# Kernel optimization log

Measured on AMD Instinct MI355X. Metric: run time of the kernel, lower is better.

## Reference

```python
import jax, jax.numpy as jnp
import numpy as np

N_SVC, N_POD, N_NODE = 2000, 8000, 1000
T, F, H = 32, 64, 128
E_SVC, E_IN, E_NI = 30000, 24000, 24000


def setup_inputs() -> dict:
    key = jax.random.key(0)
    ks = jax.random.split(key, 32)
    s = 0.05
    inp = {
        'feat_svc': jax.random.normal(ks[0], (N_SVC, T, F), jnp.float32),
        'feat_pod': jax.random.normal(ks[1], (N_POD, T, F), jnp.float32),
        'feat_node': jax.random.normal(ks[2], (N_NODE, T, F), jnp.float32),
        # per-timestep GraphConv weights (one HGraphConvLayer per window step)
        'w_svc': jax.random.normal(ks[3], (T, F, H), jnp.float32) * s,
        'b_svc': jnp.zeros((T, H), jnp.float32),
        'w_in': jax.random.normal(ks[4], (T, F, H), jnp.float32) * s,   # pod -> node
        'b_in': jnp.zeros((T, H), jnp.float32),
        'w_ni': jax.random.normal(ks[5], (T, F, H), jnp.float32) * s,   # node -> pod
        'b_ni': jnp.zeros((T, H), jnp.float32),
        # per-timestep output linears (hidden -> 1) per node type
        'lw_svc': jax.random.normal(ks[6], (T, H), jnp.float32) * s,
        'lb_svc': jnp.zeros((T,), jnp.float32),
        'lw_pod': jax.random.normal(ks[7], (T, H), jnp.float32) * s,
        'lb_pod': jnp.zeros((T,), jnp.float32),
        'lw_node': jax.random.normal(ks[8], (T, H), jnp.float32) * s,
        'lb_node': jnp.zeros((T,), jnp.float32),
        # 2-layer LSTM (input_size = T = window_simple_size)
        'w_ih0': jax.random.normal(ks[9], (4 * H, T), jnp.float32) * s,
        'w_hh0': jax.random.normal(ks[10], (4 * H, H), jnp.float32) * s,
        'b_ih0': jnp.zeros((4 * H,), jnp.float32),
        'b_hh0': jnp.zeros((4 * H,), jnp.float32),
        'w_ih1': jax.random.normal(ks[11], (4 * H, H), jnp.float32) * s,
        'w_hh1': jax.random.normal(ks[12], (4 * H, H), jnp.float32) * s,
        'b_ih1': jnp.zeros((4 * H,), jnp.float32),
        'b_hh1': jnp.zeros((4 * H,), jnp.float32),
        # heterograph edge lists
        'e_svc_src': jax.random.randint(ks[13], (E_SVC,), 0, N_SVC, jnp.int64),
        'e_svc_dst': jax.random.randint(ks[14], (E_SVC,), 0, N_SVC, jnp.int64),
        'e_in_src': jax.random.randint(ks[15], (E_IN,), 0, N_POD, jnp.int64),
        'e_in_dst': jax.random.randint(ks[16], (E_IN,), 0, N_NODE, jnp.int64),
        'e_ni_src': jax.random.randint(ks[17], (E_NI,), 0, N_NODE, jnp.int64),
        'e_ni_dst': jax.random.randint(ks[18], (E_NI,), 0, N_POD, jnp.int64),
    }
    return inp


def _graph_conv(x, src, dst, n_dst, w, b):
    # DGL GraphConv, norm='both', batched over all T timesteps at once.
    # x: [N_src, T, F], w: [T, F, H], b: [T, H] -> [N_dst, T, H]
    n_src = x.shape[0]
    ones_e = jnp.ones(src.shape[0], x.dtype)
    out_deg = jnp.clip(jax.ops.segment_sum(ones_e, src, num_segments=n_src), 1.0)
    in_deg = jnp.clip(jax.ops.segment_sum(ones_e, dst, num_segments=n_dst), 1.0)
    xs = x * (out_deg ** -0.5)[:, None, None]
    agg = jax.ops.segment_sum(xs[src], dst, num_segments=n_dst)   # [N_dst, T, F]
    agg = agg * (in_deg ** -0.5)[:, None, None]
    return jnp.einsum('ntf,tfh->nth', agg, w) + b[None]


def _leaky(v):
    return jnp.where(v >= 0, v, 0.01 * v)


def _lstm(x, w_ih, w_hh, b_ih, b_hh):
    # unbatched LSTM over leading (node) axis; PyTorch gate order i,f,g,o
    Hh = w_hh.shape[1]
    b = b_ih + b_hh
    def step(carry, xt):
        h, c = carry
        g = xt @ w_ih.T + h @ w_hh.T + b
        i, f, gg, o = jnp.split(g, 4)
        i = jax.nn.sigmoid(i); f = jax.nn.sigmoid(f)
        gg = jnp.tanh(gg); o = jax.nn.sigmoid(o)
        c = f * c + i * gg
        h = o * jnp.tanh(c)
        return (h, c), h
    init = (jnp.zeros((Hh,), x.dtype), jnp.zeros((Hh,), x.dtype))
    _, ys = jax.lax.scan(step, init, x)
    return ys


def _forward(feat_svc, feat_pod, feat_node,
             w_svc, b_svc, w_in, b_in, w_ni, b_ni,
             lw_svc, lb_svc, lw_pod, lb_pod, lw_node, lb_node,
             w_ih0, w_hh0, b_ih0, b_hh0, w_ih1, w_hh1, b_ih1, b_hh1,
             e_svc_src, e_svc_dst, e_in_src, e_in_dst, e_ni_src, e_ni_dst):
    # HeteroGraphConv (sum aggregate; each dst type receives one edge type)
    h_svc = _graph_conv(feat_svc, e_svc_src, e_svc_dst, feat_svc.shape[0], w_svc, b_svc)
    h_node = _graph_conv(feat_pod, e_in_src, e_in_dst, feat_node.shape[0], w_in, b_in)
    h_pod = _graph_conv(feat_node, e_ni_src, e_ni_dst, feat_pod.shape[0], w_ni, b_ni)
    # per-timestep LeakyReLU + Linear(hidden -> 1), per node type
    s_svc = jnp.einsum('nth,th->nt', _leaky(h_svc), lw_svc) + lb_svc[None]
    s_pod = jnp.einsum('nth,th->nt', _leaky(h_pod), lw_pod) + lb_pod[None]
    s_node = jnp.einsum('nth,th->nt', _leaky(h_node), lw_node) + lb_node[None]
    x_seq = jnp.concatenate([s_svc, s_pod, s_node], axis=0)   # [N_total, T]
    # 2-layer LSTM over the node axis, input_size = T
    y = _lstm(x_seq, w_ih0, w_hh0, b_ih0, b_hh0)
    y = _lstm(y, w_ih1, w_hh1, b_ih1, b_hh1)
    return y   # [N_total, H]


def reference(feat_svc, feat_pod, feat_node,
              w_svc, b_svc, w_in, b_in, w_ni, b_ni,
              lw_svc, lb_svc, lw_pod, lb_pod, lw_node, lb_node,
              w_ih0, w_hh0, b_ih0, b_hh0, w_ih1, w_hh1, b_ih1, b_hh1,
              e_svc_src, e_svc_dst, e_in_src, e_in_dst, e_ni_src, e_ni_dst):
    return _forward(feat_svc, feat_pod, feat_node,
                    w_svc, b_svc, w_in, b_in, w_ni, b_ni,
                    lw_svc, lb_svc, lw_pod, lb_pod, lw_node, lb_node,
                    w_ih0, w_hh0, b_ih0, b_hh0, w_ih1, w_hh1, b_ih1, b_hh1,
                    e_svc_src, e_svc_dst, e_in_src, e_in_dst, e_ni_src, e_ni_dst)
```

## Files before the change

### kernel.cpp

```cpp
#include <hip/hip_runtime.h>

#define NSVC 2000
#define NPOD 8000
#define NNODE 1000
#define NTOT 11000
#define TT 32
#define FF 64
#define HH 128
#define EA 30000
#define EB 24000
#define EC 24000
#define ETOT (EA + EB + EC)
#define CHK 64
#define NCH ((NTOT + CHK - 1) / CHK)

__device__ __forceinline__ float ld_agent(const float* p) {
    return __hip_atomic_load(p, __ATOMIC_RELAXED, __HIP_MEMORY_SCOPE_AGENT);
}
__device__ __forceinline__ void st_agent(float* p, float v) {
    __hip_atomic_store(p, v, __ATOMIC_RELAXED, __HIP_MEMORY_SCOPE_AGENT);
}
__device__ __forceinline__ void bar_fast() {
    asm volatile("s_waitcnt lgkmcnt(0)" ::: "memory");
    __builtin_amdgcn_s_barrier();
}
template<int CTRL>
__device__ __forceinline__ float qperm(float x) {
    return __int_as_float(__builtin_amdgcn_mov_dpp(__float_as_int(x), CTRL, 0xF, 0xF, false));
}

__global__ void k_count3(const int* __restrict__ sA, const int* __restrict__ dA,
                         const int* __restrict__ sB, const int* __restrict__ dB,
                         const int* __restrict__ sC, const int* __restrict__ dC,
                         float* ocA, float* icA, float* ocB, float* icB,
                         float* ocC, float* icC) {
    int e = blockIdx.x * 256 + threadIdx.x;
    if (e < EA) {
        atomicAdd(ocA + sA[e], 1.f); atomicAdd(icA + dA[e], 1.f);
    } else if (e < EA + EB) {
        int i = e - EA;
        atomicAdd(ocB + sB[i], 1.f); atomicAdd(icB + dB[i], 1.f);
    } else if (e < ETOT) {
        int i = e - EA - EB;
        atomicAdd(ocC + sC[i], 1.f); atomicAdd(icC + dC[i], 1.f);
    }
}

__global__ void k_scan(const float* cA, int nA, int* oA,
                       const float* cB, int nB, int* oB,
                       const float* cC, int nC, int* oC) {
    const float* c; int n; int* o;
    if (blockIdx.x == 0)      { c = cA; n = nA; o = oA; }
    else if (blockIdx.x == 1) { c = cB; n = nB; o = oB; }
    else                      { c = cC; n = nC; o = oC; }
    __shared__ int s[256];
    __shared__ int carry;
    int tid = threadIdx.x;
    if (tid == 0) { carry = 0; o[0] = 0; }
    __syncthreads();
    for (int base = 0; base < n; base += 256) {
        int idx = base + tid;
        int v = (idx < n) ? (int)c[idx] : 0;
        s[tid] = v;
        __syncthreads();
        for (int d = 1; d < 256; d <<= 1) {
            int t = (tid >= d) ? s[tid - d] : 0;
            __syncthreads();
            s[tid] += t;
            __syncthreads();
        }
        if (idx < n) o[idx + 1] = carry + s[tid];
        __syncthreads();
        if (tid == 255) carry += s[255];
        __syncthreads();
    }
}

__global__ void k_scatter3(const int* __restrict__ sA, const int* __restrict__ dA,
                           const int* __restrict__ sB, const int* __restrict__ dB,
                           const int* __restrict__ sC, const int* __restrict__ dC,
                           const int* offA, int* curA, int* csrA,
                           const int* offB, int* curB, int* csrB,
                           const int* offC, int* curC, int* csrC) {
    int e = blockIdx.x * 256 + threadIdx.x;
    if (e < EA) {
        int d = dA[e]; int p = atomicAdd(curA + d, 1); csrA[offA[d] + p] = sA[e];
    } else if (e < EA + EB) {
        int i = e - EA;
        int d = dB[i]; int p = atomicAdd(curB + d, 1); csrB[offB[d] + p] = sB[i];
    } else if (e < ETOT) {
        int i = e - EA - EB;
        int d = dC[i]; int p = atomicAdd(curC + d, 1); csrC[offC[d] + p] = sC[i];
    }
}

#define YA16 ((NSVC + 15) / 16)
#define YC16 ((NPOD + 15) / 16)
#define YB16 ((NNODE + 15) / 16)
__global__ __launch_bounds__(256) void k_conv3(
    const float* __restrict__ feat_svc, const float* __restrict__ feat_pod,
    const float* __restrict__ feat_node,
    const float* __restrict__ w_svc, const float* __restrict__ b_svc,
    const float* __restrict__ lw_svc, const float* __restrict__ lb_svc,
    const float* __restrict__ w_ni, const float* __restrict__ b_ni,
    const float* __restrict__ lw_pod, const float* __restrict__ lb_pod,
    const float* __restrict__ w_in, const float* __restrict__ b_in,
    const float* __restrict__ lw_node, const float* __restrict__ lb_node,
    const float* ocA, const float* icA, const int* offA, const int* csrA,
    const float* ocC, const float* icC, const int* offC, const int* csrC,
    const float* ocB, const float* icB, const int* offB, const int* csrB,
    float* __restrict__ xseq)
{
    __shared__ float wl[FF * HH];
    __shared__ float bl[HH], lwl[HH];
    __shared__ float accs[4][FF];
    const int t = blockIdx.x;
    const int tid = threadIdx.x;
    int yb = blockIdx.y;
    const float *x, *w, *b, *lw, *lb, *oc, *ic; const int *off, *csr;
    int Ndst, rowofs;
    if (yb < YA16) {
        x = feat_svc; w = w_svc; b = b_svc; lw = lw_svc; lb = lb_svc;
        oc = ocA; ic = icA; off = offA; csr = csrA; Ndst = NSVC; rowofs = 0;
    } else if (yb < YA16 + YC16) {
        yb -= YA16;
        x = feat_node; w = w_ni; b = b_ni; lw = lw_pod; lb = lb_pod;
        oc = ocC; ic = icC; off = offC; csr = csrC; Ndst = NPOD; rowofs = NSVC;
    } else {
        yb -= YA16 + YC16;
        x = feat_pod; w = w_in; b = b_in; lw = lw_node; lb = lb_node;
        oc = ocB; ic = icB; off = offB; csr = csrB; Ndst = NNODE; rowofs = NSVC + NPOD;
    }
    for (int i = tid; i < FF * HH; i += 256) wl[i] = w[t * FF * HH + i];
    if (tid < HH) { bl[tid] = b[t * HH + tid]; lwl[tid] = lw[t * HH + tid]; }
    const int wv = tid >> 6, lane = tid & 63;
    __syncthreads();
    for (int sub = 0; sub < 4; ++sub) {
        const int dstn = yb * 16 + sub * 4 + wv;
        if (dstn < Ndst) {
            float a = 0.f;
            const int e0 = off[dstn], e1 = off[dstn + 1];
            const float* xb = x + (size_t)t * FF + lane;
            float xsP = 0.f, ocP = 1.f;
            if (e0 < e1) {
                int s0 = csr[e0];
                xsP = xb[(size_t)s0 * (TT * FF)]; ocP = oc[s0];
            }
            for (int i = e0; i < e1; ++i) {
                float xs = xsP, od = ocP;
                if (i + 1 < e1) {
                    int s2 = csr[i + 1];
                    xsP = xb[(size_t)s2 * (TT * FF)]; ocP = oc[s2];
                }
                a = fmaf(xs, rsqrtf(fmaxf(od, 1.f)), a);
            }
            a *= rsqrtf(fmaxf(ic[dstn], 1.f));
            accs[wv][lane] = a;
            float h0 = bl[lane], h1v = bl[64 + lane];
            #pragma unroll
            for (int f = 0; f < FF; ++f) {
                float af = accs[wv][f];
                h0  = fmaf(af, wl[f * HH + lane], h0);
                h1v = fmaf(af, wl[f * HH + 64 + lane], h1v);
            }
            h0  = (h0  >= 0.f) ? h0  : 0.01f * h0;
            h1v = (h1v >= 0.f) ? h1v : 0.01f * h1v;
            float p = h0 * lwl[lane] + h1v * lwl[64 + lane];
            #pragma unroll
            for (int o2 = 32; o2 >= 1; o2 >>= 1) p += __shfl_down(p, o2);
            if (lane == 0) xseq[(size_t)(rowofs + dstn) * TT + t] = p + lb[t];
        }
    }
}

__device__ __forceinline__ int xcol(int r) { return ((r & 127) << 2) | (r >> 7); }

__global__ __launch_bounds__(256) void k_proj(
    const float* __restrict__ xin, int K,
    const float* __restrict__ wih,
    const float* __restrict__ bih, const float* __restrict__ bhh,
    float* __restrict__ Xout, int N)
{
    __shared__ float xt[16 * 128];
    int n0 = blockIdx.x * 16, tid = threadIdx.x;
    for (int i = tid; i < 16 * K; i += 256) {
        int nn = i / K, kk = i - nn * K;
        int n = n0 + nn;
        xt[i] = (n < N) ? xin[(size_t)n * K + kk] : 0.f;
    }
    __syncthreads();
    float acc0[16], acc1[16];
    #pragma unroll
    for (int i = 0; i < 16; ++i) { acc0[i] = 0.f; acc1[i] = 0.f; }
    int r0 = tid, r1 = tid + 256;
    for (int k = 0; k < K; ++k) {
        float w0 = wih[(size_t)r0 * K + k];
        float w1 = wih[(size_t)r1 * K + k];
        #pragma unroll
        for (int i = 0; i < 16; ++i) {
            float xv = xt[i * K + k];
            acc0[i] = fmaf(xv, w0, acc0[i]);
            acc1[i] = fmaf(xv, w1, acc1[i]);
        }
    }
    float b0 = bih[r0] + bhh[r0], b1 = bih[r1] + bhh[r1];
    int c0 = xcol(r0), c1 = xcol(r1);
    for (int i = 0; i < 16; ++i) {
        int n = n0 + i;
        if (n < N) {
            Xout[(size_t)n * 512 + c0] = acc0[i] + b0;
            Xout[(size_t)n * 512 + c1] = acc1[i] + b1;
        }
    }
}

template<bool AGX, bool AGH, bool WAIT, bool SIG>
__device__ __forceinline__ void lstm_rec(
    const float* __restrict__ X, const float* __restrict__ Whh,
    float* __restrict__ Hout, int* wflag, int* sflag)
{
    __shared__ __align__(16) float hb0s[4 * 36], hb1s[4 * 36];
    const int tid = threadIdx.x;
    const int j = tid >> 2, p = tid & 3;
    float4 w0[8], w1[8], w2[8], w3[8];
    {
        const float* bj = Whh + (size_t)j * HH + p * 32;
        const float4* r0 = reinterpret_cast<const float4*>(bj);
        const float4* r1 = reinterpret_cast<const float4*>(bj + 128 * HH);
        const float4* r2 = reinterpret_cast<const float4*>(bj + 256 * HH);
        const float4* r3 = reinterpret_cast<const float4*>(bj + 384 * HH);
        #pragma unroll
        for (int q = 0; q < 8; ++q) { w0[q]=r0[q]; w1[q]=r1[q]; w2[q]=r2[q]; w3[q]=r3[q]; }
    }
    if (tid < HH) hb0s[(tid >> 5) * 36 + (tid & 31)] = 0.f;
    const float k1 = (p == 2) ? -2.f : 1.f;
    const float k2 = (p == 2) ? 2.f : -1.f;
    const float k3 = (p == 2) ? 1.f : 0.f;
    const bool pa = (p & 1) != 0, pb = (p & 2) != 0;
    const int hst = (j >> 5) * 36 + (j & 31);
    float c = 0.f;
    __syncthreads();

#define REC_STEP(HSRC, HDST, XC, HOPTR)                                          \
    {                                                                            \
        const float4* hr = reinterpret_cast<const float4*>((HSRC) + p * 36);     \
        float s0 = 0.f, s1 = 0.f, s2 = 0.f, s3 = 0.f;                            \
        _Pragma("unroll")                                                        \
        for (int q = 0; q < 8; ++q) {                                            \
            float4 h4 = hr[q];                                                   \
            s0 = fmaf(w0[q].x, h4.x, s0); s0 = fmaf(w0[q].y, h4.y, s0);          \
            s0 = fmaf(w0[q].z, h4.z, s0); s0 = fmaf(w0[q].w, h4.w, s0);          \
            s1 = fmaf(w1[q].x, h4.x, s1); s1 = fmaf(w1[q].y, h4.y, s1);          \
            s1 = fmaf(w1[q].z, h4.z, s1); s1 = fmaf(w1[q].w, h4.w, s1);          \
            s2 = fmaf(w2[q].x, h4.x, s2); s2 = fmaf(w2[q].y, h4.y, s2);          \
            s2 = fmaf(w2[q].z, h4.z, s2); s2 = fmaf(w2[q].w, h4.w, s2);          \
            s3 = fmaf(w3[q].x, h4.x, s3); s3 = fmaf(w3[q].y, h4.y, s3);          \
            s3 = fmaf(w3[q].z, h4.z, s3); s3 = fmaf(w3[q].w, h4.w, s3);          \
        }                                                                        \
        float zA = pa ? s0 : s1;                                                 \
        float u  = (pa ? s1 : s0) + qperm<0xB1>(zA);                             \
        float zB = pa ? s2 : s3;                                                 \
        float v  = (pa ? s3 : s2) + qperm<0xB1>(zB);                             \
        float zC = pb ? u : v;                                                   \
        float sf = ((pb ? v : u) + qperm<0x4E>(zC)) + (XC);                      \
        float ev = __expf(k2 * sf);                                              \
        float a  = fmaf(k1, __builtin_amdgcn_rcpf(1.f + ev), k3);                \
        float ai = qperm<0x00>(a);                                               \
        float af = qperm<0x55>(a);                                               \
        float ag = qperm<0xAA>(a);                                               \
        float ao = qperm<0xFF>(a);                                               \
        c = fmaf(af, c, ai * ag);                                                \
        float e2 = __expf(2.f * c);                                              \
        float th = fmaf(-2.f, __builtin_amdgcn_rcpf(1.f + e2), 1.f);             \
        float hnew = ao * th;                                                    \
        if (p == 0) {                                                            \
            (HDST)[hst] = hnew;                                                  \
            if (AGH) st_agent((HOPTR), hnew); else *(HOPTR) = hnew;              \
        }                                                                        \
        bar_fast();                                                              \
    }

    for (int ch = 0; ch < NCH; ++ch) {
        const int n0 = ch * CHK;
        const int n1 = (n0 + CHK < NTOT) ? (n0 + CHK) : NTOT;
        if (WAIT) {
            if (tid == 0) {
                while (__hip_atomic_load(wflag + ch, __ATOMIC_RELAXED, __HIP_MEMORY_SCOPE_AGENT) == 0)
                    __builtin_amdgcn_s_sleep(1);
            }
            __syncthreads();
            __threadfence();
        }
        const float* xb = X + (size_t)n0 * 512 + tid;
        float* hop = Hout + (size_t)n0 * HH + j;
        float xc0 = AGX ? ld_agent(xb) : xb[0];
        float xc1 = AGX ? ld_agent(xb + 512) : xb[512];
        for (int n = n0; n < n1; n += 2) {
            float xp2 = 0.f, xp3 = 0.f;
            if (n + 2 < n1) {
                xp2 = AGX ? ld_agent(xb + 1024) : xb[1024];
                xp3 = AGX ? ld_agent(xb + 1536) : xb[1536];
            }
            REC_STEP(hb0s, hb1s, xc0, hop)
            REC_STEP(hb1s, hb0s, xc1, hop + HH)
            xc0 = xp2; xc1 = xp3;
            xb += 1024; hop += 2 * HH;
        }
        if (SIG) {
            __syncthreads();
            if (tid == 0)
                __hip_atomic_store(sflag + ch, 1, __ATOMIC_RELEASE, __HIP_MEMORY_SCOPE_AGENT);
        }
    }
#undef REC_STEP
}

__device__ __forceinline__ void proj_work(
    const float* __restrict__ h1, const float* __restrict__ Wih,
    const float* __restrict__ bih, const float* __restrict__ bhh,
    float* __restrict__ X2, int* wflag, int* sflag)
{
    __shared__ float hl[CHK * HH];
    const int tid = threadIdx.x;
    const float bsum = bih[tid] + bhh[tid];
    const int col = xcol(tid);
    const float4* wr = reinterpret_cast<const float4*>(Wih + (size_t)tid * HH);
    for (int ch = 0; ch < NCH; ++ch) {
        const int n0 = ch * CHK;
        const int cnt = (n0 + CHK < NTOT) ? CHK : (NTOT - n0);
        if (tid == 0) {
            while (__hip_atomic_load(wflag + ch, __ATOMIC_RELAXED, __HIP_MEMORY_SCOPE_AGENT) == 0)
                __builtin_amdgcn_s_sleep(1);
        }
        __syncthreads();
        __threadfence();
        for (int i = tid; i < cnt * HH; i += 512)
            hl[i] = ld_agent(h1 + (size_t)n0 * HH + i);
        __syncthreads();
        for (int t0 = 0; t0 < cnt; t0 += 16) {
            float acc[16];
            #pragma unroll
            for (int i = 0; i < 16; ++i) acc[i] = bsum;
            for (int k4 = 0; k4 < HH / 4; ++k4) {
                float4 wv = wr[k4];
                #pragma unroll
                for (int i = 0; i < 16; ++i) {
                    const float* hh = &hl[(t0 + i) * HH + 4 * k4];
                    acc[i] += wv.x*hh[0] + wv.y*hh[1] + wv.z*hh[2] + wv.w*hh[3];
                }
            }
            int tl = cnt - t0; if (tl > 16) tl = 16;
            for (int i = 0; i < tl; ++i)
                st_agent(X2 + (size_t)(n0 + t0 + i) * 512 + col, acc[i]);
        }
        __syncthreads();
        if (tid == 0)
            __hip_atomic_store(sflag + ch, 1, __ATOMIC_RELEASE, __HIP_MEMORY_SCOPE_AGENT);
    }
}

__global__ __launch_bounds__(512)
__attribute__((amdgpu_waves_per_eu(2, 2)))
void k_pipe(
    const float* __restrict__ X1, const float* __restrict__ w_hh0, float* __restrict__ h1,
    const float* __restrict__ w_ih1, const float* __restrict__ b_ih1, const float* __restrict__ b_hh1,
    float* __restrict__ X2, const float* __restrict__ w_hh1, float* __restrict__ out,
    int* flags1, int* flags2)
{
    if (blockIdx.x == 0)
        lstm_rec<false, true, false, true>(X1, w_hh0, h1, nullptr, flags1);
    else if (blockIdx.x == 1)
        proj_work(h1, w_ih1, b_ih1, b_hh1, X2, flags1, flags2);
    else
        lstm_rec<true, false, true, false>(X2, w_hh1, out, flags2, nullptr);
}

extern "C" void kernel_launch(void* const* d_in, const int* in_sizes, int n_in,
                              void* d_out, int out_size, void* d_ws, size_t ws_size,
                              hipStream_t stream) {
    const float* feat_svc = (const float*)d_in[0];
    const float* feat_pod = (const float*)d_in[1];
    const float* feat_node= (const float*)d_in[2];
    const float* w_svc = (const float*)d_in[3];
    const float* b_svc = (const float*)d_in[4];
    const float* w_in  = (const float*)d_in[5];
    const float* b_in  = (const float*)d_in[6];
    const float* w_ni  = (const float*)d_in[7];
    const float* b_ni  = (const float*)d_in[8];
    const float* lw_svc = (const float*)d_in[9];
    const float* lb_svc = (const float*)d_in[10];
    const float* lw_pod = (const float*)d_in[11];
    const float* lb_pod = (const float*)d_in[12];
    const float* lw_node= (const float*)d_in[13];
    const float* lb_node= (const float*)d_in[14];
    const float* w_ih0 = (const float*)d_in[15];
    const float* w_hh0 = (const float*)d_in[16];
    const float* b_ih0 = (const float*)d_in[17];
    const float* b_hh0 = (const float*)d_in[18];
    const float* w_ih1 = (const float*)d_in[19];
    const float* w_hh1 = (const float*)d_in[20];
    const float* b_ih1 = (const float*)d_in[21];
    const float* b_hh1 = (const float*)d_in[22];
    const int* eA_src = (const int*)d_in[23];
    const int* eA_dst = (const int*)d_in[24];
    const int* eB_src = (const int*)d_in[25];
    const int* eB_dst = (const int*)d_in[26];
    const int* eC_src = (const int*)d_in[27];
    const int* eC_dst = (const int*)d_in[28];

    float* ws = (float*)d_ws;
    float* ocA = ws + 0;
    float* icA = ws + 2000;
    float* ocB = ws + 4000;
    float* icB = ws + 12000;
    float* ocC = ws + 13000;
    float* icC = ws + 14000;
    int* curA = (int*)(ws + 22000);
    int* curB = (int*)(ws + 24000);
    int* curC = (int*)(ws + 25000);
    int* offA = (int*)(ws + 33000);
    int* offB = (int*)(ws + 35001);
    int* offC = (int*)(ws + 36002);
    int* sA   = (int*)(ws + 44003);
    int* sB   = (int*)(ws + 74003);
    int* sC   = (int*)(ws + 98003);
    float* xseq = ws + 122003;
    float* X1   = ws + 474003;
    float* h1   = ws + 6106003;
    int* flags1 = (int*)(ws + 7514003);
    int* flags2 = flags1 + NCH;
    float* X2   = X1;

    hipMemsetAsync(d_ws, 0, 33000 * sizeof(float), stream);
    hipMemsetAsync(flags1, 0, 2 * NCH * sizeof(int), stream);

    k_count3<<<(ETOT + 255) / 256, 256, 0, stream>>>(
        eA_src, eA_dst, eB_src, eB_dst, eC_src, eC_dst,
        ocA, icA, ocB, icB, ocC, icC);

    k_scan<<<3, 256, 0, stream>>>(icA, NSVC, offA, icB, NNODE, offB, icC, NPOD, offC);

    k_scatter3<<<(ETOT + 255) / 256, 256, 0, stream>>>(
        eA_src, eA_dst, eB_src, eB_dst, eC_src, eC_dst,
        offA, curA, sA, offB, curB, sB, offC, curC, sC);

    k_conv3<<<dim3(TT, YA16 + YC16 + YB16), 256, 0, stream>>>(
        feat_svc, feat_pod, feat_node,
        w_svc, b_svc, lw_svc, lb_svc,
        w_ni, b_ni, lw_pod, lb_pod,
        w_in, b_in, lw_node, lb_node,
        ocA, icA, offA, sA,
        ocC, icC, offC, sC,
        ocB, icB, offB, sB,
        xseq);

    k_proj<<<(NTOT + 15) / 16, 256, 0, stream>>>(xseq, TT, w_ih0, b_ih0, b_hh0, X1, NTOT);

    k_pipe<<<3, 512, 0, stream>>>(X1, w_hh0, h1, w_ih1, b_ih1, b_hh1,
                                  X2, w_hh1, (float*)d_out, flags1, flags2);
}
```

Baseline: 11.69 ms.

## Split LSTM recurrence dot products across 8 lanes with 1024-thread blocks

Doubles the block size of the pipelined LSTM kernel to 1024 threads. Each hidden unit's four gate dot products are now split across 8 lanes of 16 elements each instead of 4 lanes of 32, adding a ds_swizzle xor-4 reduction step. The projection worker splits its row chunks between two halves of the block. This shortens the serial per-step FMA chain on the latency-bound recurrence, at the cost of an extra cross-lane reduction, larger barriers over 16 waves, and changed register pressure under the new launch bounds.

Result: faster. 11.04 ms (-5.6%).

```diff
diff --git a/kernel.cpp b/kernel.cpp
--- a/kernel.cpp
+++ b/kernel.cpp
@@ -27,6 +27,9 @@
 template<int CTRL>
 __device__ __forceinline__ float qperm(float x) {
     return __int_as_float(__builtin_amdgcn_mov_dpp(__float_as_int(x), CTRL, 0xF, 0xF, false));
+}
+__device__ __forceinline__ float swz_xor4(float x) {
+    return __int_as_float(__builtin_amdgcn_ds_swizzle(__float_as_int(x), 0x101F));
 }
 
 __global__ void k_count3(const int* __restrict__ sA, const int* __restrict__ dA,
@@ -219,50 +222,80 @@
     const float* __restrict__ X, const float* __restrict__ Whh,
     float* __restrict__ Hout, int* wflag, int* sflag)
 {
-    __shared__ __align__(16) float hb0s[4 * 36], hb1s[4 * 36];
+    __shared__ __align__(16) float hb0s[8 * 20], hb1s[8 * 20];
     const int tid = threadIdx.x;
-    const int j = tid >> 2, p = tid & 3;
-    float4 w0[8], w1[8], w2[8], w3[8];
-    {
-        const float* bj = Whh + (size_t)j * HH + p * 32;
-        const float4* r0 = reinterpret_cast<const float4*>(bj);
-        const float4* r1 = reinterpret_cast<const float4*>(bj + 128 * HH);
-        const float4* r2 = reinterpret_cast<const float4*>(bj + 256 * HH);
-        const float4* r3 = reinterpret_cast<const float4*>(bj + 384 * HH);
-        #pragma unroll
-        for (int q = 0; q < 8; ++q) { w0[q]=r0[q]; w1[q]=r1[q]; w2[q]=r2[q]; w3[q]=r3[q]; }
-    }
-    if (tid < HH) hb0s[(tid >> 5) * 36 + (tid & 31)] = 0.f;
-    const float k1 = (p == 2) ? -2.f : 1.f;
-    const float k2 = (p == 2) ? 2.f : -1.f;
-    const float k3 = (p == 2) ? 1.f : 0.f;
+    const int j = tid >> 3, p = tid & 7;
+    const int g4 = p & 3;
+    const float* bj = Whh + (size_t)j * HH + p * 16;
+    const float4* r0 = reinterpret_cast<const float4*>(bj);
+    const float4* r1 = reinterpret_cast<const float4*>(bj + 128 * HH);
+    const float4* r2 = reinterpret_cast<const float4*>(bj + 256 * HH);
+    const float4* r3 = reinterpret_cast<const float4*>(bj + 384 * HH);
+    float4 w00 = r0[0], w01 = r0[1], w02 = r0[2], w03 = r0[3];
+    float4 w10 = r1[0], w11 = r1[1], w12 = r1[2], w13 = r1[3];
+    float4 w20 = r2[0], w21 = r2[1], w22 = r2[2], w23 = r2[3];
+    float4 w30 = r3[0], w31 = r3[1], w32 = r3[2], w33 = r3[3];
+    if (tid < 160) hb0s[tid] = 0.f;
+    const float k1 = (g4 == 2) ? -2.f : 1.f;
+    const float k2 = (g4 == 2) ? 2.f : -1.f;
+    const float k3 = (g4 == 2) ? 1.f : 0.f;
     const bool pa = (p & 1) != 0, pb = (p & 2) != 0;
-    const int hst = (j >> 5) * 36 + (j & 31);
+    const int hwr = ((j >> 4) * 20) + (j & 15);
+    const int hrd = p * 20;
+    const int xoff = (j << 2) | g4;
     float c = 0.f;
     __syncthreads();
 
 #define REC_STEP(HSRC, HDST, XC, HOPTR)                                          \
     {                                                                            \
-        const float4* hr = reinterpret_cast<const float4*>((HSRC) + p * 36);     \
-        float s0 = 0.f, s1 = 0.f, s2 = 0.f, s3 = 0.f;                            \
-        _Pragma("unroll")                                                        \
-        for (int q = 0; q < 8; ++q) {                                            \
-            float4 h4 = hr[q];                                                   \
-            s0 = fmaf(w0[q].x, h4.x, s0); s0 = fmaf(w0[q].y, h4.y, s0);          \
-            s0 = fmaf(w0[q].z, h4.z, s0); s0 = fmaf(w0[q].w, h4.w, s0);          \
-            s1 = fmaf(w1[q].x, h4.x, s1); s1 = fmaf(w1[q].y, h4.y, s1);          \
-            s1 = fmaf(w1[q].z, h4.z, s1); s1 = fmaf(w1[q].w, h4.w, s1);          \
-            s2 = fmaf(w2[q].x, h4.x, s2); s2 = fmaf(w2[q].y, h4.y, s2);          \
-            s2 = fmaf(w2[q].z, h4.z, s2); s2 = fmaf(w2[q].w, h4.w, s2);          \
-            s3 = fmaf(w3[q].x, h4.x, s3); s3 = fmaf(w3[q].y, h4.y, s3);          \
-            s3 = fmaf(w3[q].z, h4.z, s3); s3 = fmaf(w3[q].w, h4.w, s3);          \
-        }                                                                        \
+        const float4* hr = reinterpret_cast<const float4*>((HSRC) + hrd);        \
+        float4 hA = hr[0], hB = hr[1], hC = hr[2], hD = hr[3];                   \
+        float s0 = w00.x * hA.x;                                                 \
+        s0 = fmaf(w00.y, hA.y, s0); s0 = fmaf(w00.z, hA.z, s0);                  \
+        s0 = fmaf(w00.w, hA.w, s0); s0 = fmaf(w01.x, hB.x, s0);                  \
+        s0 = fmaf(w01.y, hB.y, s0); s0 = fmaf(w01.z, hB.z, s0);                  \
+        s0 = fmaf(w01.w, hB.w, s0); s0 = fmaf(w02.x, hC.x, s0);                  \
+        s0 = fmaf(w02.y, hC.y, s0); s0 = fmaf(w02.z, hC.z, s0);                  \
+        s0 = fmaf(w02.w, hC.w, s0); s0 = fmaf(w03.x, hD.x, s0);                  \
+        s0 = fmaf(w03.y, hD.y, s0); s0 = fmaf(w03.z, hD.z, s0);                  \
+        s0 = fmaf(w03.w, hD.w, s0);                                              \
+        float s1 = w10.x * hA.x;                                                 \
+        s1 = fmaf(w10.y, hA.y, s1); s1 = fmaf(w10.z, hA.z, s1);                  \
+        s1 = fmaf(w10.w, hA.w, s1); s1 = fmaf(w11.x, hB.x, s1);                  \
+        s1 = fmaf(w11.y, hB.y, s1); s1 = fmaf(w11.z, hB.z, s1);                  \
+        s1 = fmaf(w11.w, hB.w, s1); s1 = fmaf(w12.x, hC.x, s1);                  \
+        s1 = fmaf(w12.y, hC.y, s1); s1 = fmaf(w12.z, hC.z, s1);                  \
+        s1 = fmaf(w12.w, hC.w, s1); s1 = fmaf(w13.x, hD.x, s1);                  \
+        s1 = fmaf(w13.y, hD.y, s1); s1 = fmaf(w13.z, hD.z, s1);                  \
+        s1 = fmaf(w13.w, hD.w, s1);                                              \
+        float s2 = w20.x * hA.x;                                                 \
+        s2 = fmaf(w20.y, hA.y, s2); s2 = fmaf(w20.z, hA.z, s2);                  \
+        s2 = fmaf(w20.w, hA.w, s2); s2 = fmaf(w21.x, hB.x, s2);                  \
+        s2 = fmaf(w21.y, hB.y, s2); s2 = fmaf(w21.z, hB.z, s2);                  \
+        s2 = fmaf(w21.w, hB.w, s2); s2 = fmaf(w22.x, hC.x, s2);                  \
+        s2 = fmaf(w22.y, hC.y, s2); s2 = fmaf(w22.z, hC.z, s2);                  \
+        s2 = fmaf(w22.w, hC.w, s2); s2 = fmaf(w23.x, hD.x, s2);                  \
+        s2 = fmaf(w23.y, hD.y, s2); s2 = fmaf(w23.z, hD.z, s2);                  \
+        s2 = fmaf(w23.w, hD.w, s2);                                              \
+        float s3 = w30.x * hA.x;                                                 \
+        s3 = fmaf(w30.y, hA.y, s3); s3 = fmaf(w30.z, hA.z, s3);                  \
+        s3 = fmaf(w30.w, hA.w, s3); s3 = fmaf(w31.x, hB.x, s3);                  \
+        s3 = fmaf(w31.y, hB.y, s3); s3 = fmaf(w31.z, hB.z, s3);                  \
+        s3 = fmaf(w31.w, hB.w, s3); s3 = fmaf(w32.x, hC.x, s3);                  \
+        s3 = fmaf(w32.y, hC.y, s3); s3 = fmaf(w32.z, hC.z, s3);                  \
+        s3 = fmaf(w32.w, hC.w, s3); s3 = fmaf(w33.x, hD.x, s3);                  \
+        s3 = fmaf(w33.y, hD.y, s3); s3 = fmaf(w33.z, hD.z, s3);                  \
+        s3 = fmaf(w33.w, hD.w, s3);                                              \
+           \
         float zA = pa ? s0 : s1;                                                 \
         float u  = (pa ? s1 : s0) + qperm<0xB1>(zA);                             \
         float zB = pa ? s2 : s3;                                                 \
         float v  = (pa ? s3 : s2) + qperm<0xB1>(zB);                             \
         float zC = pb ? u : v;                                                   \
-        float sf = ((pb ? v : u) + qperm<0x4E>(zC)) + (XC);                      \
+        float sf = (pb ? v : u) + qperm<0x4E>(zC);                               \
+             \
+        sf += swz_xor4(sf);                                                      \
+        sf += (XC);                                                              \
         float ev = __expf(k2 * sf);                                              \
         float a  = fmaf(k1, __builtin_amdgcn_rcpf(1.f + ev), k3);                \
         float ai = qperm<0x00>(a);                                               \
@@ -274,7 +307,7 @@
         float th = fmaf(-2.f, __builtin_amdgcn_rcpf(1.f + e2), 1.f);             \
         float hnew = ao * th;                                                    \
         if (p == 0) {                                                            \
-            (HDST)[hst] = hnew;                                                  \
+            (HDST)[hwr] = hnew;                                                  \
             if (AGH) st_agent((HOPTR), hnew); else *(HOPTR) = hnew;              \
         }                                                                        \
         bar_fast();                                                              \
@@ -291,7 +324,7 @@
             __syncthreads();
             __threadfence();
         }
-        const float* xb = X + (size_t)n0 * 512 + tid;
+        const float* xb = X + (size_t)n0 * 512 + xoff;
         float* hop = Hout + (size_t)n0 * HH + j;
         float xc0 = AGX ? ld_agent(xb) : xb[0];
         float xc1 = AGX ? ld_agent(xb + 512) : xb[512];
@@ -322,9 +355,11 @@
 {
     __shared__ float hl[CHK * HH];
     const int tid = threadIdx.x;
-    const float bsum = bih[tid] + bhh[tid];
-    const int col = xcol(tid);
-    const float4* wr = reinterpret_cast<const float4*>(Wih + (size_t)tid * HH);
+    const int r = tid & 511;
+    const int half = tid >> 9;
+    const float bsum = bih[r] + bhh[r];
+    const int col = xcol(r);
+    const float4* wr = reinterpret_cast<const float4*>(Wih + (size_t)r * HH);
     for (int ch = 0; ch < NCH; ++ch) {
         const int n0 = ch * CHK;
         const int cnt = (n0 + CHK < NTOT) ? CHK : (NTOT - n0);
@@ -334,10 +369,10 @@
         }
         __syncthreads();
         __threadfence();
-        for (int i = tid; i < cnt * HH; i += 512)
+        for (int i = tid; i < cnt * HH; i += 1024)
             hl[i] = ld_agent(h1 + (size_t)n0 * HH + i);
         __syncthreads();
-        for (int t0 = 0; t0 < cnt; t0 += 16) {
+        for (int t0 = half * 16; t0 < cnt; t0 += 32) {
             float acc[16];
             #pragma unroll
             for (int i = 0; i < 16; ++i) acc[i] = bsum;
@@ -359,9 +394,7 @@
     }
 }
 
-__global__ __launch_bounds__(512)
-__attribute__((amdgpu_waves_per_eu(2, 2)))
-void k_pipe(
+__global__ __launch_bounds__(1024, 4) void k_pipe(
     const float* __restrict__ X1, const float* __restrict__ w_hh0, float* __restrict__ h1,
     const float* __restrict__ w_ih1, const float* __restrict__ b_ih1, const float* __restrict__ b_hh1,
     float* __restrict__ X2, const float* __restrict__ w_hh1, float* __restrict__ out,
@@ -456,6 +489,6 @@
 
     k_proj<<<(NTOT + 15) / 16, 256, 0, stream>>>(xseq, TT, w_ih0, b_ih0, b_hh0, X1, NTOT);
 
-    k_pipe<<<3, 512, 0, stream>>>(X1, w_hh0, h1, w_ih1, b_ih1, b_hh1,
-                                  X2, w_hh1, (float*)d_out, flags1, flags2);
-}
+    k_pipe<<<3, 1024, 0, stream>>>(X1, w_hh0, h1, w_ih1, b_ih1, b_hh1,
+                                   X2, w_hh1, (float*)d_out, flags1, flags2);
+}
```
